# Performance work log

Measured on AMD Instinct MI355X. Metric: run time of the kernel, lower is better.

Reference implementation:

```python
import jax, jax.numpy as jnp
import numpy as np


def setup_inputs() -> dict:
    key = jax.random.key(0)
    inputs = jax.random.normal(key, (32, 8192, 128), dtype=jnp.float32)
    return {"inputs": inputs}


def reference(inputs):
    # Per-batch covariance, matching tfp.stats.covariance defaults:
    # sample_axis=0 (here axis 1 per batch item), event_axis=-1, divide by N.
    n = inputs.shape[1]
    mean = jnp.mean(inputs, axis=1, keepdims=True)          # [B, 1, D]
    xc = inputs - mean                                       # [B, N, D]
    cov = jnp.einsum('bnd,bne->bde', xc, xc) / n             # [B, D, D]
    return cov
```

## Files before the change

kernel.cpp:

```cpp
#include <hip/hip_runtime.h>

#define D_DIM 128
#define N_DIM 8192
#define B_DIM 32
#define KSPL 32
#define KC   256
#define BK   128

typedef float f32x4 __attribute__((ext_vector_type(4)));
typedef short bf16x8 __attribute__((ext_vector_type(8)));
typedef unsigned short u16;

__device__ __forceinline__ u16 f2bf(float f) {
    unsigned int u = __builtin_bit_cast(unsigned int, f);
    u += 0x7FFFu + ((u >> 16) & 1u);
    return (u16)(u >> 16);
}

__device__ __forceinline__ void load_chunk(f32x4 (&buf)[8], const float* src,
                                           int gc, int nr, int dc) {
    const float* p = src + (size_t)gc * 64 * D_DIM;
#pragma unroll
    for (int sub = 0; sub < 2; ++sub)
#pragma unroll
        for (int i = 0; i < 4; ++i)
            buf[sub * 4 + i] =
                *(const f32x4*)(p + (size_t)(sub * 32 + 4 * nr + i) * D_DIM + 4 * dc);
}

__device__ __forceinline__ void proc_write(u16* lds, f32x4 (&buf)[8],
                                           float (&sum4)[4], int gc, int nr, int dc) {
#pragma unroll
    for (int x = 0; x < 8; ++x)
#pragma unroll
        for (int j = 0; j < 4; ++j) sum4[j] += buf[x][j];
#pragma unroll
    for (int sub = 0; sub < 2; ++sub)
#pragma unroll
        for (int j = 0; j < 4; ++j) {
            ushort4 w;
            w.x = f2bf(buf[sub * 4 + 0][j]);
            w.y = f2bf(buf[sub * 4 + 1][j]);
            w.z = f2bf(buf[sub * 4 + 2][j]);
            w.w = f2bf(buf[sub * 4 + 3][j]);
            int d = 4 * dc + j;
            int g = (gc & 1) * 8 + sub * 4 + (nr >> 1);
            int slot = g ^ (d & 7);
            *(ushort4*)(lds + d * 128 + slot * 8 + 4 * (nr & 1)) = w;
        }
}

__device__ __forceinline__ void mfma_phase(const u16* lds, f32x4 (&acc)[2][8],
                                           int wv, int m, int q) {
#pragma unroll
    for (int h = 0; h < 4; ++h) {
        int slotbase = h * 4 + q;
        bf16x8 Fcol[8];
#pragma unroll
        for (int tt = 0; tt < 8; ++tt) {
            int slot = slotbase ^ (m & 7);
            Fcol[tt] = *(const bf16x8*)(lds + (16 * tt + m) * 128 + slot * 8);
        }
        bf16x8 Frow0, Frow1;
        {
            int slot = slotbase ^ (m & 7);
            Frow0 = *(const bf16x8*)(lds + (32 * wv + m) * 128 + slot * 8);
            Frow1 = *(const bf16x8*)(lds + (32 * wv + 16 + m) * 128 + slot * 8);
        }
#pragma unroll
        for (int c = 0; c < 8; ++c)
            acc[0][c] = __builtin_amdgcn_mfma_f32_16x16x32_bf16(Frow0, Fcol[c],
                                                                acc[0][c], 0, 0, 0);
#pragma unroll
        for (int c = 0; c < 8; ++c)
            acc[1][c] = __builtin_amdgcn_mfma_f32_16x16x32_bf16(Frow1, Fcol[c],
                                                                acc[1][c], 0, 0, 0);
    }
}

__global__ __launch_bounds__(256) void cov_partial(
    const float* __restrict__ in, float* __restrict__ ws_p,
    float* __restrict__ ws_s) {
    __shared__ u16 lds[D_DIM * BK];
    __shared__ float red[8][D_DIM];

    const int t    = threadIdx.x;
    const int b    = blockIdx.y;
    const int ks   = blockIdx.x;
    const int dc   = t >> 3;
    const int nr   = t & 7;
    const int wv   = t >> 6;
    const int lane = t & 63;
    const int m    = lane & 15;
    const int q    = lane >> 4;

    const float* src = in + (size_t)b * (N_DIM * D_DIM) + (size_t)ks * KC * D_DIM;

    f32x4 acc[2][8];
#pragma unroll
    for (int r = 0; r < 2; ++r)
#pragma unroll
        for (int c = 0; c < 8; ++c) acc[r][c] = (f32x4)0.0f;
    float sum4[4] = {0.f, 0.f, 0.f, 0.f};

    f32x4 bufA[8], bufB[8];

    load_chunk(bufA, src, 0, nr, dc);
    load_chunk(bufB, src, 1, nr, dc);
    proc_write(lds, bufA, sum4, 0, nr, dc);
    proc_write(lds, bufB, sum4, 1, nr, dc);
    __syncthreads();
    mfma_phase(lds, acc, wv, m, q);
    __syncthreads();

    load_chunk(bufA, src, 2, nr, dc);
    load_chunk(bufB, src, 3, nr, dc);
    proc_write(lds, bufA, sum4, 2, nr, dc);
    proc_write(lds, bufB, sum4, 3, nr, dc);
    __syncthreads();
    mfma_phase(lds, acc, wv, m, q);

    __syncthreads();
#pragma unroll
    for (int j = 0; j < 4; ++j) red[nr][4 * dc + j] = sum4[j];
    __syncthreads();
    if (t < D_DIM) {
        float ssum = 0.f;
#pragma unroll
        for (int i = 0; i < 8; ++i) ssum += red[i][t];
        ws_s[(size_t)(b * KSPL + ks) * D_DIM + t] = ssum;
    }

    f32x4* outv = (f32x4*)(ws_p + (size_t)(b * KSPL + ks) * (D_DIM * D_DIM));
#pragma unroll
    for (int r = 0; r < 2; ++r)
#pragma unroll
        for (int c = 0; c < 8; ++c)
            outv[t * 16 + r * 8 + c] = acc[r][c];
}

__global__ __launch_bounds__(256) void cov_reduce(
    const float* __restrict__ ws_p, const float* __restrict__ ws_s,
    float* __restrict__ out, int kspl) {
    int b = blockIdx.x >> 4;
    int chunk = blockIdx.x & 15;
    int g = chunk * 256 + threadIdx.x;

    __shared__ float mean[D_DIM];
    if (threadIdx.x < D_DIM) {
        float s = 0.f;
        for (int ks = 0; ks < kspl; ++ks)
            s += ws_s[(size_t)(b * kspl + ks) * D_DIM + threadIdx.x];
        mean[threadIdx.x] = s * (1.0f / (float)N_DIM);
    }
    __syncthreads();

    const f32x4* pv = (const f32x4*)ws_p;
    f32x4 acc = (f32x4)0.0f;
    for (int ks = 0; ks < kspl; ++ks) {
        f32x4 v = pv[(size_t)(b * kspl + ks) * (D_DIM * D_DIM / 4) + g];
        acc.x += v.x; acc.y += v.y; acc.z += v.z; acc.w += v.w;
    }

    int t2 = g >> 4;
    int rc = g & 15;
    int r = rc >> 3, c = rc & 7;
    int wv = t2 >> 6;
    int lane = t2 & 63;
    int m = lane & 15;
    int q = lane >> 4;
    int d0 = 32 * wv + 16 * r + 4 * q;
    int e = 16 * c + m;

    const float invN = 1.0f / (float)N_DIM;
    float me = mean[e];
    float* ob = out + (size_t)b * (D_DIM * D_DIM);
#pragma unroll
    for (int i = 0; i < 4; ++i) {
        int d = d0 + i;
        ob[(size_t)d * D_DIM + e] = acc[i] * invN - mean[d] * me;
    }
}

extern "C" void kernel_launch(void* const* d_in, const int* in_sizes, int n_in,
                              void* d_out, int out_size, void* d_ws, size_t ws_size,
                              hipStream_t stream) {
    const float* in = (const float*)d_in[0];
    float* out = (float*)d_out;

    float* ws_p = (float*)d_ws;
    float* ws_s = ws_p + (size_t)KSPL * B_DIM * (D_DIM * D_DIM);

    cov_partial<<<dim3(KSPL, B_DIM), 256, 0, stream>>>(in, ws_p, ws_s);
    cov_reduce<<<dim3(B_DIM * 16), 256, 0, stream>>>(ws_p, ws_s, out, KSPL);
}
```

Baseline: 229.9 us.

## Stage input via async global_load_lds and overlap loads with MFMA phase

Replaces register-staged global loads with direct global-to-LDS loads into two fp32 staging buffers using a swizzled layout. A four-pass loop converts staged fp32 to a smaller 64-wide bf16 tile, then issues the next chunk's async loads before running the MFMA phase, so memory traffic overlaps compute. This adds LDS use for the staging buffers and more barriers per pass, and relies on the barrier to cover completion of the async loads.

```diff
diff --git a/kernel.cpp b/kernel.cpp
--- a/kernel.cpp
+++ b/kernel.cpp
@@ -5,11 +5,13 @@
 #define B_DIM 32
 #define KSPL 32
 #define KC   256
-#define BK   128
 
 typedef float f32x4 __attribute__((ext_vector_type(4)));
 typedef short bf16x8 __attribute__((ext_vector_type(8)));
 typedef unsigned short u16;
+
+using gvp = const __attribute__((address_space(1))) void*;
+using lvp = __attribute__((address_space(3))) void*;
 
 __device__ __forceinline__ u16 f2bf(float f) {
     unsigned int u = __builtin_bit_cast(unsigned int, f);
@@ -17,56 +19,57 @@
     return (u16)(u >> 16);
 }
 
-__device__ __forceinline__ void load_chunk(f32x4 (&buf)[8], const float* src,
-                                           int gc, int nr, int dc) {
-    const float* p = src + (size_t)gc * 64 * D_DIM;
-#pragma unroll
-    for (int sub = 0; sub < 2; ++sub)
-#pragma unroll
-        for (int i = 0; i < 4; ++i)
-            buf[sub * 4 + i] =
-                *(const f32x4*)(p + (size_t)(sub * 32 + 4 * nr + i) * D_DIM + 4 * dc);
-}
-
-__device__ __forceinline__ void proc_write(u16* lds, f32x4 (&buf)[8],
-                                           float (&sum4)[4], int gc, int nr, int dc) {
-#pragma unroll
-    for (int x = 0; x < 8; ++x)
-#pragma unroll
-        for (int j = 0; j < 4; ++j) sum4[j] += buf[x][j];
-#pragma unroll
-    for (int sub = 0; sub < 2; ++sub)
-#pragma unroll
-        for (int j = 0; j < 4; ++j) {
-            ushort4 w;
-            w.x = f2bf(buf[sub * 4 + 0][j]);
-            w.y = f2bf(buf[sub * 4 + 1][j]);
-            w.z = f2bf(buf[sub * 4 + 2][j]);
-            w.w = f2bf(buf[sub * 4 + 3][j]);
-            int d = 4 * dc + j;
-            int g = (gc & 1) * 8 + sub * 4 + (nr >> 1);
-            int slot = g ^ (d & 7);
-            *(ushort4*)(lds + d * 128 + slot * 8 + 4 * (nr & 1)) = w;
-        }
-}
-
-__device__ __forceinline__ void mfma_phase(const u16* lds, f32x4 (&acc)[2][8],
-                                           int wv, int m, int q) {
-#pragma unroll
-    for (int h = 0; h < 4; ++h) {
-        int slotbase = h * 4 + q;
+__device__ __forceinline__ void stage_issue(const float* gsrc_chunk, float* stage,
+                                            int wv, int lane) {
+    const int half = lane >> 5;
+    const int sl   = lane & 31;
+#pragma unroll
+    for (int i = 0; i < 4; ++i) {
+        int kl = 8 * wv + 2 * i + half;
+        int gg = sl ^ (kl & 31);
+        const float* gp = gsrc_chunk + (size_t)kl * D_DIM + gg * 4;
+        float* lp = stage + (8 * wv + 2 * i) * D_DIM;
+        __builtin_amdgcn_global_load_lds((gvp)gp, (lvp)lp, 16, 0, 0);
+    }
+}
+
+__device__ __forceinline__ void pass2_chunk(const float* stage, u16* tile,
+                                            float (&sum4)[4], int c ,
+                                            int nr, int dc) {
+    f32x4 v[4];
+#pragma unroll
+    for (int i = 0; i < 4; ++i) {
+        int kl = 4 * nr + i;
+        int slot = (dc ^ kl) & 31;
+        v[i] = *(const f32x4*)(stage + (size_t)kl * D_DIM + slot * 4);
+    }
+#pragma unroll
+    for (int i = 0; i < 4; ++i)
+#pragma unroll
+        for (int j = 0; j < 4; ++j) sum4[j] += v[i][j];
+#pragma unroll
+    for (int j = 0; j < 4; ++j) {
+        ushort4 w;
+        w.x = f2bf(v[0][j]); w.y = f2bf(v[1][j]);
+        w.z = f2bf(v[2][j]); w.w = f2bf(v[3][j]);
+        int d = 4 * dc + j;
+        int g = c * 4 + (nr >> 1);
+        int slot = g ^ (d & 7);
+        *(ushort4*)(tile + d * 64 + slot * 8 + 4 * (nr & 1)) = w;
+    }
+}
+
+__device__ __forceinline__ void mfma_phase64(const u16* tile, f32x4 (&acc)[2][8],
+                                             int wv, int m, int q) {
+#pragma unroll
+    for (int h = 0; h < 2; ++h) {
+        int slot = (4 * h + q) ^ (m & 7);
         bf16x8 Fcol[8];
 #pragma unroll
-        for (int tt = 0; tt < 8; ++tt) {
-            int slot = slotbase ^ (m & 7);
-            Fcol[tt] = *(const bf16x8*)(lds + (16 * tt + m) * 128 + slot * 8);
-        }
-        bf16x8 Frow0, Frow1;
-        {
-            int slot = slotbase ^ (m & 7);
-            Frow0 = *(const bf16x8*)(lds + (32 * wv + m) * 128 + slot * 8);
-            Frow1 = *(const bf16x8*)(lds + (32 * wv + 16 + m) * 128 + slot * 8);
-        }
+        for (int tt = 0; tt < 8; ++tt)
+            Fcol[tt] = *(const bf16x8*)(tile + (16 * tt + m) * 64 + slot * 8);
+        bf16x8 Frow0 = *(const bf16x8*)(tile + (32 * wv + m) * 64 + slot * 8);
+        bf16x8 Frow1 = *(const bf16x8*)(tile + (32 * wv + 16 + m) * 64 + slot * 8);
 #pragma unroll
         for (int c = 0; c < 8; ++c)
             acc[0][c] = __builtin_amdgcn_mfma_f32_16x16x32_bf16(Frow0, Fcol[c],
@@ -81,7 +84,9 @@
 __global__ __launch_bounds__(256) void cov_partial(
     const float* __restrict__ in, float* __restrict__ ws_p,
     float* __restrict__ ws_s) {
-    __shared__ u16 lds[D_DIM * BK];
+    __shared__ float stg0[32 * D_DIM];
+    __shared__ float stg1[32 * D_DIM];
+    __shared__ u16 tile[D_DIM * 64];
     __shared__ float red[8][D_DIM];
 
     const int t    = threadIdx.x;
@@ -103,24 +108,23 @@
         for (int c = 0; c < 8; ++c) acc[r][c] = (f32x4)0.0f;
     float sum4[4] = {0.f, 0.f, 0.f, 0.f};
 
-    f32x4 bufA[8], bufB[8];
-
-    load_chunk(bufA, src, 0, nr, dc);
-    load_chunk(bufB, src, 1, nr, dc);
-    proc_write(lds, bufA, sum4, 0, nr, dc);
-    proc_write(lds, bufB, sum4, 1, nr, dc);
+    stage_issue(src, stg0, wv, lane);
+    stage_issue(src + 32 * D_DIM, stg1, wv, lane);
     __syncthreads();
-    mfma_phase(lds, acc, wv, m, q);
-    __syncthreads();
-
-    load_chunk(bufA, src, 2, nr, dc);
-    load_chunk(bufB, src, 3, nr, dc);
-    proc_write(lds, bufA, sum4, 2, nr, dc);
-    proc_write(lds, bufB, sum4, 3, nr, dc);
-    __syncthreads();
-    mfma_phase(lds, acc, wv, m, q);
-
-    __syncthreads();
+
+    for (int p = 0; p < 4; ++p) {
+        pass2_chunk(stg0, tile, sum4, 0, nr, dc);
+        pass2_chunk(stg1, tile, sum4, 1, nr, dc);
+        __syncthreads();
+
+        if (p < 3) {
+            stage_issue(src + (size_t)(2 * p + 2) * 32 * D_DIM, stg0, wv, lane);
+            stage_issue(src + (size_t)(2 * p + 3) * 32 * D_DIM, stg1, wv, lane);
+        }
+        mfma_phase64(tile, acc, wv, m, q);
+        __syncthreads();
+    }
+
 #pragma unroll
     for (int j = 0; j < 4; ++j) red[nr][4 * dc + j] = sum4[j];
     __syncthreads();
```

After: 226.2 us. Within noise of the previous version (-1.6%).
